# Performance work log

Hardware: AMD Instinct MI355X
Metric: run time of the kernel (lower is better)

The kernel has to match this reference:

```python
import jax, jax.numpy as jnp
import numpy as np

B, S, D, H = 1, 3072, 2048, 16
HD = D // H          # head_dim = 128
C = HD // 2          # rotary complex pairs = 64
EPS = 1e-6
WINDOW = 3           # frames of sliding-window attention on each side
L_TOKENS = 256       # tokens per frame (forward arg L)
NUM_FRAMES = S // L_TOKENS


def setup_inputs() -> dict:
    key = jax.random.key(0)
    ks = jax.random.split(key, 5)
    scale = 1.0 / np.sqrt(D)
    x = jax.random.normal(ks[0], (B, S, D), jnp.float32)
    wq = jax.random.normal(ks[1], (D, D), jnp.float32) * scale
    wk = jax.random.normal(ks[2], (D, D), jnp.float32) * scale
    wv = jax.random.normal(ks[3], (D, D), jnp.float32) * scale
    wo = jax.random.normal(ks[4], (D, D), jnp.float32) * scale
    bq = jnp.zeros((D,), jnp.float32)
    bk = jnp.zeros((D,), jnp.float32)
    bv = jnp.zeros((D,), jnp.float32)
    bo = jnp.zeros((D,), jnp.float32)
    gq = jnp.ones((D,), jnp.float32)
    gk = jnp.ones((D,), jnp.float32)
    # rotary freqs as cos/sin of angle t * theta_c (source uses a complex [S,1,C] tensor)
    t = jnp.arange(S, dtype=jnp.float32)
    inv_freq = 1.0 / (10000.0 ** (jnp.arange(C, dtype=jnp.float32) / C))
    ang = t[:, None] * inv_freq[None, :]        # [S, C]
    cos = jnp.cos(ang)[:, None, :]              # [S, 1, C]
    sin = jnp.sin(ang)[:, None, :]              # [S, 1, C]
    return {"x": x, "wq": wq, "bq": bq, "wk": wk, "bk": bk, "wv": wv,
            "bv": bv, "wo": wo, "bo": bo, "gq": gq, "gk": gk,
            "cos": cos, "sin": sin, "f": NUM_FRAMES, "L": L_TOKENS}


def _rms_norm(h, g, eps=EPS):
    # tensor_parallel_rms_norm with tp_size=1: fp32 variance, rsqrt, scale by weight
    hf = h.astype(jnp.float32)
    var = jnp.mean(hf * hf, axis=-1, keepdims=True)
    return (hf * jax.lax.rsqrt(var + eps) * g).astype(h.dtype)


def _rope(h, cos, sin):
    # complex rotation on interleaved (real, imag) pairs per head (rope_apply_for3d)
    b, s, d = h.shape
    hd = 2 * cos.shape[-1]
    n = d // hd
    hr = h.reshape(b, s, n, hd)
    xr, xi = hr[..., 0::2], hr[..., 1::2]       # [b,s,n,C]
    c, sn = cos[None], sin[None]                # [1,s,1,C] broadcast over heads
    yr = xr * c - xi * sn
    yi = xr * sn + xi * c
    y = jnp.stack([yr, yi], axis=-1).reshape(b, s, n, hd)
    return y.reshape(b, s, d)


def reference(x, wq, bq, wk, bk, wv, bv, wo, bo, gq, gk, cos, sin, f, L):
    q = _rope(_rms_norm(x @ wq.T + bq, gq), cos, sin)
    k = _rope(_rms_norm(x @ wk.T + bk, gk), cos, sin)
    v = x @ wv.T + bv
    b, s, d = q.shape
    hd = 2 * cos.shape[-1]
    n = d // hd
    qh = q.reshape(b, s, n, hd)
    kh = k.reshape(b, s, n, hd)
    vh = v.reshape(b, s, n, hd)
    scale = 1.0 / np.sqrt(hd)
    scores = jnp.einsum('bqnd,bknd->bnqk', qh, kh) * scale
    win = L * WINDOW
    idx = jnp.arange(s)
    delta = idx[None, :] - idx[:, None]
    mask = (delta <= win) & (delta >= -win)
    scores = jnp.where(mask[None, None], scores, -jnp.inf)
    probs = jax.nn.softmax(scores, axis=-1)
    out = jnp.einsum('bnqk,bknd->bqnd', probs, vh).reshape(b, s, d)
    return out @ wo.T + bo
```

## Files before the change

### kernel.cpp

```cpp
#include <hip/hip_runtime.h>
#include <stdint.h>

typedef unsigned short u16;
typedef __attribute__((ext_vector_type(8))) short short8;
typedef __attribute__((ext_vector_type(4))) float f32x4;

#define S_LEN 3072
#define D_DIM 2048
#define WIN 768
#define INV_SQRT_HD 0.08838834764831845f
#define M_SHIFT 12.0f

__device__ __forceinline__ u16 f2bf(float x) {
  union { float f; uint32_t u; } v; v.f = x;
  uint32_t r = v.u + 0x7FFFu + ((v.u >> 16) & 1u);
  return (u16)(r >> 16);
}
__device__ __forceinline__ float bf2f(u16 x) {
  union { uint32_t u; float f; } v; v.u = ((uint32_t)x) << 16;
  return v.f;
}

__device__ __forceinline__ void load_lds16(const void* g, void* l) {
  __builtin_amdgcn_global_load_lds(
      (const __attribute__((address_space(1))) void*)g,
      (__attribute__((address_space(3))) void*)l, 16, 0, 0);
}

#define MFMA16(a, b, c) __builtin_amdgcn_mfma_f32_16x16x32_bf16((a), (b), (c), 0, 0, 0)

__global__ __launch_bounds__(256) void k_cvt_all(const float* __restrict__ x,
                                                 const float* __restrict__ w0, const float* __restrict__ w1,
                                                 const float* __restrict__ w2, const float* __restrict__ w3,
                                                 u16* __restrict__ xo,
                                                 u16* __restrict__ o0, u16* __restrict__ o1,
                                                 u16* __restrict__ o2, u16* __restrict__ o3,
                                                 int n4x, int n4w) {
  int i = blockIdx.x * 256 + threadIdx.x;
  const float* in;
  u16* out;
  int off;
  if (i < n4x) {
    in = x; out = xo; off = i;
  } else {
    int j = i - n4x;
    int seg = j / n4w;
    off = j - seg * n4w;
    in = seg == 0 ? w0 : seg == 1 ? w1 : seg == 2 ? w2 : w3;
    out = seg == 0 ? o0 : seg == 1 ? o1 : seg == 2 ? o2 : o3;
  }
  float4 v = ((const float4*)in)[off];
  ushort4 o;
  o.x = f2bf(v.x); o.y = f2bf(v.y); o.z = f2bf(v.z); o.w = f2bf(v.w);
  ((ushort4*)out)[off] = o;
}

__device__ __forceinline__ void gemm_body(const u16* __restrict__ A, const u16* __restrict__ B,
                                          int m0, int n0, int t, f32x4 (*acc)[4],
                                          u16* lA, u16* lB) {
  const int lane = t & 63, w = t >> 6, lo = lane & 15, g = lane >> 4;
  const int wr = w >> 1, wc = w & 1;
  const int srow = t >> 2;
  const int sch = (t & 3) ^ ((srow ^ (srow >> 3)) & 3);
  const u16* ga = A + (size_t)(m0 + srow) * D_DIM + sch * 8;
  const u16* gb = B + (size_t)(n0 + srow) * D_DIM + sch * 8;
  for (int k0 = 0; k0 < D_DIM; k0 += 32) {
    load_lds16(ga + k0, &lA[t * 8]);
    load_lds16(ga + (size_t)64 * D_DIM + k0, &lA[2048 + t * 8]);
    load_lds16(gb + k0, &lB[t * 8]);
    load_lds16(gb + (size_t)64 * D_DIM + k0, &lB[2048 + t * 8]);
    __syncthreads();
    short8 af[4], bfr[4];
#pragma unroll
    for (int m = 0; m < 4; ++m) {
      const int R = wr * 64 + m * 16 + lo;
      af[m] = *(const short8*)&lA[R * 32 + ((g ^ ((R ^ (R >> 3)) & 3)) << 3)];
    }
#pragma unroll
    for (int n = 0; n < 4; ++n) {
      const int R = wc * 64 + n * 16 + lo;
      bfr[n] = *(const short8*)&lB[R * 32 + ((g ^ ((R ^ (R >> 3)) & 3)) << 3)];
    }
#pragma unroll
    for (int m = 0; m < 4; ++m)
#pragma unroll
      for (int n = 0; n < 4; ++n) acc[m][n] = MFMA16(af[m], bfr[n], acc[m][n]);
    __syncthreads();
  }
}

__global__ __launch_bounds__(256) void k_gemm_qkv(const u16* __restrict__ A,
                                                  const u16* __restrict__ Bq, const u16* __restrict__ Bk,
                                                  const u16* __restrict__ Bv,
                                                  const float* __restrict__ bq, const float* __restrict__ bk,
                                                  const float* __restrict__ bv,
                                                  u16* __restrict__ Qb, u16* __restrict__ Kb,
                                                  u16* __restrict__ Vb) {
  __shared__ u16 lA[128 * 32];
  __shared__ u16 lB[128 * 32];
  const int id = blockIdx.x;
  const int xcd = id & 7, local = id >> 3;
  const int m_idx = xcd * 3 + local / 48;
  const int n_idx = local % 48;
  const int m0 = m_idx * 128;
  const int seg = n_idx >> 4, n0 = (n_idx & 15) * 128;
  const u16* B = seg == 0 ? Bq : seg == 1 ? Bk : Bv;
  const float* bias = seg == 0 ? bq : seg == 1 ? bk : bv;
  u16* D = seg == 0 ? Qb : seg == 1 ? Kb : Vb;
  const int t = threadIdx.x;
  const int lane = t & 63, w = t >> 6, lo = lane & 15, g = lane >> 4;
  const int wr = w >> 1, wc = w & 1;
  const f32x4 zero4 = {0.f, 0.f, 0.f, 0.f};
  f32x4 acc[4][4];
#pragma unroll
  for (int m = 0; m < 4; ++m)
#pragma unroll
    for (int n = 0; n < 4; ++n) acc[m][n] = zero4;
  gemm_body(A, B, m0, n0, t, acc, lA, lB);
#pragma unroll
  for (int m = 0; m < 4; ++m) {
    const int row = m0 + wr * 64 + m * 16 + 4 * g;
#pragma unroll
    for (int n = 0; n < 4; ++n) {
      const int col = n0 + wc * 64 + n * 16 + lo;
      const float bb = bias[col];
#pragma unroll
      for (int r = 0; r < 4; ++r)
        D[(size_t)(row + r) * 2048 + col] = f2bf(acc[m][n][r] + bb);
    }
  }
}

__global__ __launch_bounds__(256) void k_gemm_wo(const u16* __restrict__ A,
                                                 const u16* __restrict__ B,
                                                 const float* __restrict__ bias,
                                                 float* __restrict__ C) {
  __shared__ u16 lA[128 * 32];
  __shared__ u16 lB[128 * 32];
  const int id = blockIdx.x;
  const int xcd = id & 7, local = id >> 3;
  const int m_idx = xcd * 3 + local / 16;
  const int n_idx = local % 16;
  const int m0 = m_idx * 128, n0 = n_idx * 128;
  const int t = threadIdx.x;
  const int lane = t & 63, w = t >> 6, lo = lane & 15, g = lane >> 4;
  const int wr = w >> 1, wc = w & 1;
  const f32x4 zero4 = {0.f, 0.f, 0.f, 0.f};
  f32x4 acc[4][4];
#pragma unroll
  for (int m = 0; m < 4; ++m)
#pragma unroll
    for (int n = 0; n < 4; ++n) acc[m][n] = zero4;
  gemm_body(A, B, m0, n0, t, acc, lA, lB);
#pragma unroll
  for (int m = 0; m < 4; ++m) {
    const int row = m0 + wr * 64 + m * 16 + 4 * g;
#pragma unroll
    for (int n = 0; n < 4; ++n) {
      const int col = n0 + wc * 64 + n * 16 + lo;
      const float bb = bias[col];
#pragma unroll
      for (int r = 0; r < 4; ++r)
        C[(size_t)(row + r) * 2048 + col] = acc[m][n][r] + bb;
    }
  }
}

__global__ __launch_bounds__(256) void k_rms_rope2(const u16* __restrict__ Q0, const u16* __restrict__ K0,
                                                   const float* __restrict__ gq, const float* __restrict__ gk,
                                                   const float* __restrict__ cosT, const float* __restrict__ sinT,
                                                   u16* __restrict__ qo, u16* __restrict__ ko) {
  const int s = blockIdx.x, t = threadIdx.x;
  const u16* H = blockIdx.y ? K0 : Q0;
  const float* gain = blockIdx.y ? gk : gq;
  u16* out = blockIdx.y ? ko : qo;
  const short8 hv = *(const short8*)(H + (size_t)s * D_DIM + t * 8);
  float h[8];
#pragma unroll
  for (int j = 0; j < 8; ++j) h[j] = bf2f((u16)hv[j]);
  float ss = 0.f;
#pragma unroll
  for (int j = 0; j < 8; ++j) ss += h[j] * h[j];
#pragma unroll
  for (int off = 32; off > 0; off >>= 1) ss += __shfl_xor(ss, off);
  __shared__ float red[4];
  if ((t & 63) == 0) red[t >> 6] = ss;
  __syncthreads();
  ss = red[0] + red[1] + red[2] + red[3];
  const float rs = rsqrtf(ss * (1.f / D_DIM) + 1e-6f);
  const float4 g0 = *(const float4*)(gain + t * 8);
  const float4 g1 = *(const float4*)(gain + t * 8 + 4);
  float y[8];
  y[0] = h[0] * rs * g0.x; y[1] = h[1] * rs * g0.y;
  y[2] = h[2] * rs * g0.z; y[3] = h[3] * rs * g0.w;
  y[4] = h[4] * rs * g1.x; y[5] = h[5] * rs * g1.y;
  y[6] = h[6] * rs * g1.z; y[7] = h[7] * rs * g1.w;
  const int cbase = ((t * 8) & 127) >> 1;
  short8 o8;
#pragma unroll
  for (int i = 0; i < 4; ++i) {
    const float cs = cosT[s * 64 + cbase + i];
    const float sn = sinT[s * 64 + cbase + i];
    const float yr = y[2 * i] * cs - y[2 * i + 1] * sn;
    const float yi = y[2 * i] * sn + y[2 * i + 1] * cs;
    o8[2 * i] = (short)f2bf(yr);
    o8[2 * i + 1] = (short)f2bf(yi);
  }
  *(short8*)(out + (size_t)s * D_DIM + t * 8) = o8;
}

__global__ __launch_bounds__(256) void k_transpose(const u16* __restrict__ in,
                                                   u16* __restrict__ out) {
  __shared__ u16 tile[64][72];
  const int s0 = blockIdx.x * 64, d0 = blockIdx.y * 64;
  const int t = threadIdx.x;
  const int r = t >> 3, c8 = (t & 7) * 8;
#pragma unroll
  for (int p = 0; p < 2; ++p) {
    short8 v = *(const short8*)&in[(size_t)(s0 + r + p * 32) * D_DIM + d0 + c8];
#pragma unroll
    for (int j = 0; j < 8; ++j) tile[r + p * 32][c8 + j] = (u16)v[j];
  }
  __syncthreads();
#pragma unroll
  for (int p = 0; p < 2; ++p) {
    const int dr = r + p * 32;
    short8 o;
#pragma unroll
    for (int j = 0; j < 8; ++j) o[j] = (short)tile[c8 + j][dr];
    *(short8*)&out[(size_t)(d0 + dr) * S_LEN + s0 + c8] = o;
  }
}

__global__ __launch_bounds__(256, 3) void k_attn5(const u16* __restrict__ Q,
                                                  const u16* __restrict__ Kmat,
                                                  const u16* __restrict__ Vt,
                                                  u16* __restrict__ Oa,
                                                  u16* __restrict__ Ob,
                                                  float* __restrict__ lbuf) {
  const int qt = blockIdx.x, h = blockIdx.y, z = blockIdx.z;
  const int t = threadIdx.x, w = t >> 6, lane = t & 63, lo = lane & 15, g = lane >> 4;
  const int q0 = qt * 128;
  const int wrow = q0 + w * 32;
  const size_t hoff = (size_t)h * 128;

  __shared__ u16 lK[2][32 * 128];
  __shared__ u16 lV[2][128 * 32];
  __shared__ u16 ldsp[4][32][40];

  short8 qf[2][4];
#pragma unroll
  for (int m = 0; m < 2; ++m) {
    const u16* qp = Q + (size_t)(wrow + m * 16 + lo) * D_DIM + hoff + g * 8;
#pragma unroll
    for (int c = 0; c < 4; ++c) qf[m][c] = *(const short8*)(qp + c * 32);
  }

  const f32x4 zero4 = {0.f, 0.f, 0.f, 0.f};
  f32x4 oacc[2][8];
#pragma unroll
  for (int m = 0; m < 2; ++m)
#pragma unroll
    for (int ct = 0; ct < 8; ++ct) oacc[m][ct] = zero4;
  float lrun[2][4] = {{0.f, 0.f, 0.f, 0.f}, {0.f, 0.f, 0.f, 0.f}};

  int jlo = q0 - WIN; if (jlo < 0) jlo = 0;
  int jhi = q0 + 127 + WIN + 1; if (jhi > S_LEN) jhi = S_LEN;
  const int NT = (jhi - jlo) >> 5;
  const int it0 = z * (NT >> 1), it1 = it0 + (NT >> 1);

  const int krow = t >> 4,          kch  = (t & 15) ^ (krow & 7);
  const int krow1 = (t + 256) >> 4, kch1 = (t & 15) ^ (krow1 & 7);
  const int vrow = t >> 2,          vch  = (t & 3) ^ ((vrow >> 1) & 3);
  const int vrow1 = (t + 256) >> 2, vch1 = (t & 3) ^ ((vrow1 >> 1) & 3);

#define STAGE5(buf, jj)                                                                              \
  do {                                                                                               \
    load_lds16(Kmat + (size_t)((jj) + krow) * D_DIM + hoff + (kch << 3), &lK[buf][t * 8]);           \
    load_lds16(Kmat + (size_t)((jj) + krow1) * D_DIM + hoff + (kch1 << 3), &lK[buf][(t + 256) * 8]); \
    load_lds16(Vt + (size_t)(hoff + vrow) * S_LEN + (jj) + (vch << 3), &lV[buf][t * 8]);             \
    load_lds16(Vt + (size_t)(hoff + vrow1) * S_LEN + (jj) + (vch1 << 3), &lV[buf][(t + 256) * 8]);   \
  } while (0)

  STAGE5(0, jlo + (it0 << 5));
  __syncthreads();
  int cur = 0;
  for (int it = it0; it < it1; ++it) {
    const int j0 = jlo + (it << 5);
    if (it + 1 < it1) STAGE5(cur ^ 1, j0 + 32);

    f32x4 sc[2][2];
    sc[0][0] = zero4; sc[0][1] = zero4; sc[1][0] = zero4; sc[1][1] = zero4;
#pragma unroll
    for (int half = 0; half < 2; ++half) {
#pragma unroll
      for (int c = 0; c < 4; ++c) {
        const short8 kf = *(const short8*)
            &lK[cur][(half * 16 + lo) * 128 + (((g + 4 * c) ^ (lo & 7)) << 3)];
        sc[0][half] = MFMA16(qf[0][c], kf, sc[0][half]);
        sc[1][half] = MFMA16(qf[1][c], kf, sc[1][half]);
      }
    }

    const int dq = j0 - q0;
    const bool interior = (dq >= -640) && (dq <= 736);
#pragma unroll
    for (int m = 0; m < 2; ++m) {
#pragma unroll
      for (int r = 0; r < 4; ++r) {
        float a0 = fmaf(sc[m][0][r], INV_SQRT_HD, -M_SHIFT);
        float a1 = fmaf(sc[m][1][r], INV_SQRT_HD, -M_SHIFT);
        if (!interior) {
          const int dk = j0 + lo - (wrow + m * 16 + 4 * g + r);
          if (dk < -WIN || dk > WIN) a0 = -3e38f;
          if (dk + 16 < -WIN || dk + 16 > WIN) a1 = -3e38f;
        }
        const float p0 = __expf(a0);
        const float p1 = __expf(a1);
        lrun[m][r] += p0 + p1;
        ldsp[w][m * 16 + 4 * g + r][lo] = f2bf(p0);
        ldsp[w][m * 16 + 4 * g + r][16 + lo] = f2bf(p1);
      }
    }

    const short8 pf0 = *(const short8*)&ldsp[w][lo][g * 8];
    const short8 pf1 = *(const short8*)&ldsp[w][16 + lo][g * 8];
#pragma unroll
    for (int ct = 0; ct < 8; ++ct) {
      const short8 vf = *(const short8*)
          &lV[cur][(ct * 16 + lo) * 32 + ((g ^ ((lo >> 1) & 3)) << 3)];
      oacc[0][ct] = MFMA16(pf0, vf, oacc[0][ct]);
      oacc[1][ct] = MFMA16(pf1, vf, oacc[1][ct]);
    }
    __syncthreads();
    cur ^= 1;
  }
#undef STAGE5

#pragma unroll
  for (int off = 8; off > 0; off >>= 1)
#pragma unroll
    for (int m = 0; m < 2; ++m)
#pragma unroll
      for (int r = 0; r < 4; ++r) lrun[m][r] += __shfl_xor(lrun[m][r], off);

  u16* Op = z ? Ob : Oa;
#pragma unroll
  for (int m = 0; m < 2; ++m)
#pragma unroll
    for (int r = 0; r < 4; ++r) {
      const int row = wrow + m * 16 + 4 * g + r;
#pragma unroll
      for (int ct = 0; ct < 8; ++ct)
        Op[(size_t)row * D_DIM + hoff + ct * 16 + lo] = f2bf(oacc[m][ct][r]);
      if (lo == 0) lbuf[(size_t)z * S_LEN * 16 + (size_t)row * 16 + h] = lrun[m][r];
    }
}

__global__ __launch_bounds__(256) void k_combine(const u16* __restrict__ Oa,
                                                 const u16* __restrict__ Ob,
                                                 const float* __restrict__ lbuf,
                                                 u16* __restrict__ out) {
  const int i = blockIdx.x * 256 + threadIdx.x;
  const int s = i >> 8, d8 = (i & 255) * 8, h = d8 >> 7;
  const float la = lbuf[(size_t)s * 16 + h];
  const float lb = lbuf[(size_t)S_LEN * 16 + (size_t)s * 16 + h];
  const float inv = 1.f / (la + lb);
  const size_t base = (size_t)s * D_DIM + d8;
  const short8 a = *(const short8*)(Oa + base);
  const short8 b = *(const short8*)(Ob + base);
  short8 o;
#pragma unroll
  for (int j = 0; j < 8; ++j)
    o[j] = (short)f2bf((bf2f((u16)a[j]) + bf2f((u16)b[j])) * inv);
  *(short8*)(out + base) = o;
}

extern "C" void kernel_launch(void* const* d_in, const int* in_sizes, int n_in,
                              void* d_out, int out_size, void* d_ws, size_t ws_size,
                              hipStream_t stream) {
  const float* x    = (const float*)d_in[0];
  const float* wq   = (const float*)d_in[1];
  const float* bq   = (const float*)d_in[2];
  const float* wk   = (const float*)d_in[3];
  const float* bk   = (const float*)d_in[4];
  const float* wv   = (const float*)d_in[5];
  const float* bv   = (const float*)d_in[6];
  const float* wo   = (const float*)d_in[7];
  const float* bo   = (const float*)d_in[8];
  const float* gq   = (const float*)d_in[9];
  const float* gk   = (const float*)d_in[10];
  const float* cosT = (const float*)d_in[11];
  const float* sinT = (const float*)d_in[12];

  char* ws = (char*)d_ws;
  const size_t WB = (size_t)D_DIM * D_DIM * 2;
  const size_t XB = (size_t)S_LEN * D_DIM * 2;
  u16*   wq_bf = (u16*)(ws);
  u16*   wk_bf = (u16*)(ws + WB);
  u16*   wv_bf = (u16*)(ws + 2 * WB);
  u16*   wo_bf = (u16*)(ws + 3 * WB);
  u16*   x_bf  = (u16*)(ws + 4 * WB);
  u16*   Q0b   = (u16*)(ws + 4 * WB + XB);
  u16*   K0b   = (u16*)(ws + 4 * WB + 2 * XB);
  u16*   V0b   = (u16*)(ws + 4 * WB + 3 * XB);
  float* lbuf  = (float*)(ws + 4 * WB + 4 * XB);
  u16* q_bf = x_bf;
  u16* k_bf = wq_bf;
  u16* vT   = Q0b;
  u16* Ob   = K0b;
  u16* Oa   = (u16*)d_out;
  u16* attn = V0b;

  const int nw4 = (D_DIM * D_DIM) / 4;
  const int nx4 = (S_LEN * D_DIM) / 4;
  k_cvt_all<<<(nx4 + 4 * nw4) / 256, 256, 0, stream>>>(
      x, wq, wk, wv, wo, x_bf, wq_bf, wk_bf, wv_bf, wo_bf, nx4, nw4);

  k_gemm_qkv<<<1152, 256, 0, stream>>>(x_bf, wq_bf, wk_bf, wv_bf, bq, bk, bv, Q0b, K0b, V0b);

  k_rms_rope2<<<dim3(S_LEN, 2), 256, 0, stream>>>(Q0b, K0b, gq, gk, cosT, sinT, q_bf, k_bf);
  k_transpose<<<dim3(S_LEN / 64, D_DIM / 64), 256, 0, stream>>>(V0b, vT);

  k_attn5<<<dim3(S_LEN / 128, 16, 2), 256, 0, stream>>>(q_bf, k_bf, vT, Oa, Ob, lbuf);
  k_combine<<<(S_LEN * D_DIM / 8) / 256, 256, 0, stream>>>(Oa, Ob, lbuf, attn);

  k_gemm_wo<<<384, 256, 0, stream>>>(attn, wo_bf, bo, (float*)d_out);
}
```

Measured before the change: 256.0 us.

## Fuse QKV weights into one 128x192-tile GEMM with concatenated bias

```diff
diff --git a/kernel.cpp b/kernel.cpp
--- a/kernel.cpp
+++ b/kernel.cpp
@@ -32,27 +32,106 @@
 __global__ __launch_bounds__(256) void k_cvt_all(const float* __restrict__ x,
                                                  const float* __restrict__ w0, const float* __restrict__ w1,
                                                  const float* __restrict__ w2, const float* __restrict__ w3,
+                                                 const float* __restrict__ bq, const float* __restrict__ bk,
+                                                 const float* __restrict__ bv,
                                                  u16* __restrict__ xo,
                                                  u16* __restrict__ o0, u16* __restrict__ o1,
                                                  u16* __restrict__ o2, u16* __restrict__ o3,
+                                                 float* __restrict__ bias_all,
                                                  int n4x, int n4w) {
   int i = blockIdx.x * 256 + threadIdx.x;
-  const float* in;
-  u16* out;
-  int off;
-  if (i < n4x) {
-    in = x; out = xo; off = i;
+  if (i < n4x + 4 * n4w) {
+    const float* in;
+    u16* out;
+    int off;
+    if (i < n4x) {
+      in = x; out = xo; off = i;
+    } else {
+      int j = i - n4x;
+      int seg = j / n4w;
+      off = j - seg * n4w;
+      in = seg == 0 ? w0 : seg == 1 ? w1 : seg == 2 ? w2 : w3;
+      out = seg == 0 ? o0 : seg == 1 ? o1 : seg == 2 ? o2 : o3;
+    }
+    float4 v = ((const float4*)in)[off];
+    ushort4 o;
+    o.x = f2bf(v.x); o.y = f2bf(v.y); o.z = f2bf(v.z); o.w = f2bf(v.w);
+    ((ushort4*)out)[off] = o;
   } else {
-    int j = i - n4x;
-    int seg = j / n4w;
-    off = j - seg * n4w;
-    in = seg == 0 ? w0 : seg == 1 ? w1 : seg == 2 ? w2 : w3;
-    out = seg == 0 ? o0 : seg == 1 ? o1 : seg == 2 ? o2 : o3;
-  }
-  float4 v = ((const float4*)in)[off];
-  ushort4 o;
-  o.x = f2bf(v.x); o.y = f2bf(v.y); o.z = f2bf(v.z); o.w = f2bf(v.w);
-  ((ushort4*)out)[off] = o;
+    int j = i - n4x - 4 * n4w;
+    int seg = j >> 9, off = j & 511;
+    const float* in = seg == 0 ? bq : seg == 1 ? bk : bv;
+    ((float4*)bias_all)[j] = ((const float4*)in)[off];
+  }
+}
+
+__global__ __launch_bounds__(256, 3) void k_gemm_qkv(const u16* __restrict__ A,
+                                                     const u16* __restrict__ Ball,
+                                                     const float* __restrict__ bias_all,
+                                                     u16* __restrict__ QKV) {
+  __shared__ u16 lA[128 * 32];
+  __shared__ u16 lB[192 * 32];
+  const int id = blockIdx.x;
+  const int xcd = id & 7, local = id >> 3;
+  const int m_idx = xcd * 3 + local / 32;
+  const int n_idx = local % 32;
+  const int m0 = m_idx * 128;
+  const int n0g = n_idx * 192;
+  const int t = threadIdx.x;
+  const int lane = t & 63, w = t >> 6, lo = lane & 15, g = lane >> 4;
+  const int wr = w >> 1, wc = w & 1;
+
+  const int srow = t >> 2;
+  const int sch = (t & 3) ^ ((srow ^ (srow >> 3)) & 3);
+  const u16* ga = A + (size_t)(m0 + srow) * D_DIM + sch * 8;
+  const u16* gb = Ball + (size_t)(n0g + srow) * D_DIM + sch * 8;
+
+  const f32x4 zero4 = {0.f, 0.f, 0.f, 0.f};
+  f32x4 acc[4][6];
+#pragma unroll
+  for (int m = 0; m < 4; ++m)
+#pragma unroll
+    for (int n = 0; n < 6; ++n) acc[m][n] = zero4;
+
+  for (int k0 = 0; k0 < D_DIM; k0 += 32) {
+    load_lds16(ga + k0, &lA[t * 8]);
+    load_lds16(ga + (size_t)64 * D_DIM + k0, &lA[2048 + t * 8]);
+    load_lds16(gb + k0, &lB[t * 8]);
+    load_lds16(gb + (size_t)64 * D_DIM + k0, &lB[2048 + t * 8]);
+    load_lds16(gb + (size_t)128 * D_DIM + k0, &lB[4096 + t * 8]);
+    __syncthreads();
+    short8 af[4], bfr[6];
+#pragma unroll
+    for (int m = 0; m < 4; ++m) {
+      const int R = wr * 64 + m * 16 + lo;
+      af[m] = *(const short8*)&lA[R * 32 + ((g ^ ((R ^ (R >> 3)) & 3)) << 3)];
+    }
+#pragma unroll
+    for (int n = 0; n < 6; ++n) {
+      const int R = wc * 96 + n * 16 + lo;
+      bfr[n] = *(const short8*)&lB[R * 32 + ((g ^ ((R ^ (R >> 3)) & 3)) << 3)];
+    }
+#pragma unroll
+    for (int m = 0; m < 4; ++m)
+#pragma unroll
+      for (int n = 0; n < 6; ++n) acc[m][n] = MFMA16(af[m], bfr[n], acc[m][n]);
+    __syncthreads();
+  }
+
+#pragma unroll
+  for (int m = 0; m < 4; ++m) {
+    const int row = m0 + wr * 64 + m * 16 + 4 * g;
+#pragma unroll
+    for (int n = 0; n < 6; ++n) {
+      const int col_g = n0g + wc * 96 + n * 16 + lo;
+      const int seg_c = col_g >> 11, c = col_g & 2047;
+      u16* D = QKV + (size_t)seg_c * S_LEN * D_DIM;
+      const float bb = bias_all[col_g];
+#pragma unroll
+      for (int r = 0; r < 4; ++r)
+        D[(size_t)(row + r) * D_DIM + c] = f2bf(acc[m][n][r] + bb);
+    }
+  }
 }
 
 __device__ __forceinline__ void gemm_body(const u16* __restrict__ A, const u16* __restrict__ B,
@@ -89,48 +168,6 @@
   }
 }
 
-__global__ __launch_bounds__(256) void k_gemm_qkv(const u16* __restrict__ A,
-                                                  const u16* __restrict__ Bq, const u16* __restrict__ Bk,
-                                                  const u16* __restrict__ Bv,
-                                                  const float* __restrict__ bq, const float* __restrict__ bk,
-                                                  const float* __restrict__ bv,
-                                                  u16* __restrict__ Qb, u16* __restrict__ Kb,
-                                                  u16* __restrict__ Vb) {
-  __shared__ u16 lA[128 * 32];
-  __shared__ u16 lB[128 * 32];
-  const int id = blockIdx.x;
-  const int xcd = id & 7, local = id >> 3;
-  const int m_idx = xcd * 3 + local / 48;
-  const int n_idx = local % 48;
-  const int m0 = m_idx * 128;
-  const int seg = n_idx >> 4, n0 = (n_idx & 15) * 128;
-  const u16* B = seg == 0 ? Bq : seg == 1 ? Bk : Bv;
-  const float* bias = seg == 0 ? bq : seg == 1 ? bk : bv;
-  u16* D = seg == 0 ? Qb : seg == 1 ? Kb : Vb;
-  const int t = threadIdx.x;
-  const int lane = t & 63, w = t >> 6, lo = lane & 15, g = lane >> 4;
-  const int wr = w >> 1, wc = w & 1;
-  const f32x4 zero4 = {0.f, 0.f, 0.f, 0.f};
-  f32x4 acc[4][4];
-#pragma unroll
-  for (int m = 0; m < 4; ++m)
-#pragma unroll
-    for (int n = 0; n < 4; ++n) acc[m][n] = zero4;
-  gemm_body(A, B, m0, n0, t, acc, lA, lB);
-#pragma unroll
-  for (int m = 0; m < 4; ++m) {
-    const int row = m0 + wr * 64 + m * 16 + 4 * g;
-#pragma unroll
-    for (int n = 0; n < 4; ++n) {
-      const int col = n0 + wc * 64 + n * 16 + lo;
-      const float bb = bias[col];
-#pragma unroll
-      for (int r = 0; r < 4; ++r)
-        D[(size_t)(row + r) * 2048 + col] = f2bf(acc[m][n][r] + bb);
-    }
-  }
-}
-
 __global__ __launch_bounds__(256) void k_gemm_wo(const u16* __restrict__ A,
                                                  const u16* __restrict__ B,
                                                  const float* __restrict__ bias,
@@ -405,6 +442,7 @@
   u16*   K0b   = (u16*)(ws + 4 * WB + 2 * XB);
   u16*   V0b   = (u16*)(ws + 4 * WB + 3 * XB);
   float* lbuf  = (float*)(ws + 4 * WB + 4 * XB);
+  float* bias_all = (float*)(ws + 4 * WB + 4 * XB + 512 * 1024);
   u16* q_bf = x_bf;
   u16* k_bf = wq_bf;
   u16* vT   = Q0b;
@@ -414,10 +452,11 @@
 
   const int nw4 = (D_DIM * D_DIM) / 4;
   const int nx4 = (S_LEN * D_DIM) / 4;
-  k_cvt_all<<<(nx4 + 4 * nw4) / 256, 256, 0, stream>>>(
-      x, wq, wk, wv, wo, x_bf, wq_bf, wk_bf, wv_bf, wo_bf, nx4, nw4);
-
-  k_gemm_qkv<<<1152, 256, 0, stream>>>(x_bf, wq_bf, wk_bf, wv_bf, bq, bk, bv, Q0b, K0b, V0b);
+  const int ncvt = nx4 + 4 * nw4 + 6144 / 4;
+  k_cvt_all<<<ncvt / 256, 256, 0, stream>>>(
+      x, wq, wk, wv, wo, bq, bk, bv, x_bf, wq_bf, wk_bf, wv_bf, wo_bf, bias_all, nx4, nw4);
+
+  k_gemm_qkv<<<768, 256, 0, stream>>>(x_bf, wq_bf, bias_all, Q0b);
 
   k_rms_rope2<<<dim3(S_LEN, 2), 256, 0, stream>>>(Q0b, K0b, gq, gk, cosT, sinT, q_bf, k_bf);
   k_transpose<<<dim3(S_LEN / 64, D_DIM / 64), 256, 0, stream>>>(V0b, vT);
```

New measurement: 228.8 us. 1.12x faster.
